# Kernel tuning notes

Measured on AMD Instinct MI355X. Metric: run time of the kernel, lower is better.

Reference implementation:

```python
import jax, jax.numpy as jnp
import numpy as np

S, R, NUM_LORA = 16384, 64, 8
NQ, NKV = 4096, 1024
OUT_DIM = NQ + 2 * NKV
BS, MAX_LEN = 32, 512


def setup_inputs() -> dict:
    key = jax.random.key(0)
    k1, k2, k3, k4, k5, k6 = jax.random.split(key, 6)
    x = jax.random.normal(k1, (S, 3 * R), dtype=jnp.float32)
    qkv_lora_b = jax.random.normal(k2, (NUM_LORA, OUT_DIM, R), dtype=jnp.float32) * 0.02
    seg_indptr = (jnp.arange(BS + 1, dtype=jnp.int32) * MAX_LEN)
    seg_lens = jax.random.randint(k3, (BS,), 256, MAX_LEN + 1, dtype=jnp.int32)
    weight_indices = jax.random.randint(k4, (BS,), 0, NUM_LORA, dtype=jnp.int32)
    # ranks in [0, R]; rank 0 means the segment is a no-op
    lora_ranks = jax.random.randint(k5, (NUM_LORA,), 0, R + 1, dtype=jnp.int32)
    scalings = jax.random.uniform(k6, (NUM_LORA,), minval=0.25, maxval=2.0, dtype=jnp.float32)
    output_offset = jnp.array([0, NQ, NQ + NKV, OUT_DIM], dtype=jnp.int32)
    return {
        "x": x,
        "qkv_lora_b": qkv_lora_b,
        "use_cuda_graph": False,
        "bs": BS,
        "num_segments": BS,
        "seg_indptr": seg_indptr,
        "weight_indices": weight_indices,
        "lora_ranks": lora_ranks,
        "scalings": scalings,
        "max_len": MAX_LEN,
        "seg_lens": seg_lens,
        "permutation": jnp.arange(BS, dtype=jnp.int32),
        "output_offset": output_offset,
        "max_qkv_out_dim": NQ,
    }


def _qkv_lora_b(x, qkv_lora_b, bs, seg_indptr, weight_indices, lora_ranks,
                scalings, max_len, seg_lens, offs):
    s = x.shape[0]
    out_dim, r = qkv_lora_b.shape[1], qkv_lora_b.shape[2]
    L = max_len
    w_idx = weight_indices[:bs]                      # (bs,)
    W = qkv_lora_b[w_idx]                            # (bs, out_dim, r)
    keff = jnp.minimum(r, lora_ranks[w_idx])         # effective rank per segment
    scale = scalings[w_idx]                          # (bs,)
    # gather padded per-segment token blocks
    pos = seg_indptr[:bs, None] + jnp.arange(L, dtype=seg_indptr.dtype)[None, :]   # (bs, L)
    valid = jnp.arange(L)[None, :] < seg_lens[:bs, None]                            # (bs, L)
    Xp = jnp.where(valid[..., None], x[jnp.clip(pos, 0, s - 1)], 0.0)               # (bs, L, 3r)
    # x columns for qkv slice q are [q*keff, q*keff + keff) (packed with stride keff)
    kidx = jnp.arange(r, dtype=jnp.int32)
    cols = jnp.arange(3, dtype=jnp.int32)[None, :, None] * keff[:, None, None] + kidx[None, None, :]  # (bs,3,r)
    kmask = kidx[None, None, :] < keff[:, None, None]
    cols = jnp.where(kmask, cols, 0)
    Xg = jnp.take_along_axis(Xp[:, :, None, :],
                             jnp.broadcast_to(cols[:, None], (bs, L, 3, r)), axis=3)  # (bs, L, 3, r)
    Xg = Xg * kmask[:, None].astype(Xg.dtype)
    # 3 packed GEMMs against the statically-partitioned B weight (Q / K / V rows)
    parts = [jnp.einsum('blk,bnk->bln', Xg[:, :, q], W[:, offs[q]:offs[q + 1], :])
             for q in range(3)]
    seg_out = jnp.concatenate(parts, axis=-1) * scale[:, None, None]    # (bs, L, out_dim)
    # masked scatter-add back into the flat output buffer
    pos_safe = jnp.where(valid, pos, s)   # out-of-range index -> dropped
    out = jnp.zeros((s, out_dim), dtype=x.dtype)
    out = out.at[pos_safe.reshape(-1)].add(seg_out.reshape(-1, out_dim), mode='drop')
    return out


def reference(x, qkv_lora_b, use_cuda_graph, bs, num_segments, seg_indptr,
              weight_indices, lora_ranks, scalings, max_len, seg_lens,
              permutation, output_offset, max_qkv_out_dim):
    offs = np.asarray(jax.device_get(output_offset))  # static [0, Nq, Nq+Nkv, out_dim]
    return _qkv_lora_b(x, qkv_lora_b, int(bs), seg_indptr, weight_indices,
                       lora_ranks, scalings, int(max_len), seg_lens, offs)
```

## Files before the change

### kernel.cpp

```cpp
#include <hip/hip_runtime.h>
#include <stddef.h>

#define SROWS   16384
#define ODIM    6144
#define RMAX    64
#define SEGLEN  512
#define TM      64
#define TN      128
#define XDIM    192

typedef float f4_t __attribute__((ext_vector_type(4)));

__global__ __launch_bounds__(256, 3) void lora_qkv_b_kernel(
    const float* __restrict__ x,
    const float* __restrict__ w_all,
    const int*   __restrict__ weight_indices,
    const int*   __restrict__ lora_ranks,
    const float* __restrict__ scalings,
    const int*   __restrict__ seg_lens,
    float*       __restrict__ out)
{
    __shared__ float xs[TM][RMAX];
    __shared__ float wlds[RMAX][TN + 4];

    const int seg   = blockIdx.x;
    const int cb    = blockIdx.y;
    const int half  = blockIdx.z;
    const int n0    = cb * TN;
    const int segbase = seg * SEGLEN;
    const int lbase = half * (SEGLEN / 2);

    const int w    = weight_indices[seg];
    int keff       = lora_ranks[w];
    if (keff > RMAX) keff = RMAX;
    const float scale = scalings[w];
    const int slen    = seg_lens[seg];

    const int tid    = threadIdx.x;
    const int rbase  = (tid >> 5) * 8;
    const int nlocal = (tid & 31) * 4;

    if (keff == 0 || lbase >= slen) {
        const f4_t z = (f4_t)0.f;
        for (int c = 0; c < 4; ++c) {
            const int i0 = segbase + lbase + c * TM;
            #pragma unroll
            for (int r = 0; r < 8; ++r)
                __builtin_nontemporal_store(
                    z, (f4_t*)(out + (size_t)(i0 + rbase + r) * ODIM + n0 + nlocal));
        }
        return;
    }

    const int q    = (n0 < 4096) ? 0 : ((n0 < 5120) ? 1 : 2);
    const int qoff = q * keff;
    const float* Wb = w_all + ((size_t)w * ODIM + n0) * RMAX;

    for (int idx = tid * 4; idx < TN * RMAX; idx += 256 * 4) {
        const int n  = idx >> 6;
        const int k0 = idx & 63;
        float4 v = make_float4(0.f, 0.f, 0.f, 0.f);
        if (k0 < keff) {
            v = *(const float4*)(Wb + (size_t)n * RMAX + k0);
            if (k0 + 1 >= keff) v.y = 0.f;
            if (k0 + 2 >= keff) v.z = 0.f;
            if (k0 + 3 >= keff) v.w = 0.f;
        }
        wlds[k0 + 0][n] = v.x;
        wlds[k0 + 1][n] = v.y;
        wlds[k0 + 2][n] = v.z;
        wlds[k0 + 3][n] = v.w;
    }

    const int kk = tid & 63;
    const int r0 = tid >> 6;
    const int keff4 = (keff + 3) & ~3;

    float pref[16];
    {
        const float* p = x + ((size_t)(segbase + lbase) + r0) * XDIM + qoff + kk;
        #pragma unroll
        for (int m = 0; m < 16; ++m) pref[m] = p[(size_t)m * 4 * XDIM];
    }

    for (int c = 0; c < 4; ++c) {
        const int l0 = lbase + c * TM;
        const int i0 = segbase + l0;

        if (l0 >= slen) {
            const f4_t z = (f4_t)0.f;
            #pragma unroll
            for (int r = 0; r < 8; ++r)
                __builtin_nontemporal_store(
                    z, (f4_t*)(out + (size_t)(i0 + rbase + r) * ODIM + n0 + nlocal));
            continue;
        }

        if (l0 + TM <= slen) {
            #pragma unroll
            for (int m = 0; m < 16; ++m) xs[m * 4 + r0][kk] = pref[m];
        } else {
            #pragma unroll
            for (int m = 0; m < 16; ++m)
                xs[m * 4 + r0][kk] = (l0 + m * 4 + r0 < slen) ? pref[m] : 0.f;
        }

        __syncthreads();

        if (c < 3 && l0 + TM < slen) {
            const float* p = x + ((size_t)(i0 + TM) + r0) * XDIM + qoff + kk;
            #pragma unroll
            for (int m = 0; m < 16; ++m) pref[m] = p[(size_t)m * 4 * XDIM];
        }

        float acc[8][4];
        #pragma unroll
        for (int r = 0; r < 8; ++r)
            #pragma unroll
            for (int cc = 0; cc < 4; ++cc) acc[r][cc] = 0.f;

        for (int k = 0; k < keff4; k += 4) {
            const float4 w0 = *(const float4*)(&wlds[k + 0][nlocal]);
            const float4 w1 = *(const float4*)(&wlds[k + 1][nlocal]);
            const float4 w2 = *(const float4*)(&wlds[k + 2][nlocal]);
            const float4 w3 = *(const float4*)(&wlds[k + 3][nlocal]);
            #pragma unroll
            for (int r = 0; r < 8; ++r) {
                const float4 xv = *(const float4*)(&xs[rbase + r][k]);
                acc[r][0] += xv.x * w0.x; acc[r][1] += xv.x * w0.y;
                acc[r][2] += xv.x * w0.z; acc[r][3] += xv.x * w0.w;
                acc[r][0] += xv.y * w1.x; acc[r][1] += xv.y * w1.y;
                acc[r][2] += xv.y * w1.z; acc[r][3] += xv.y * w1.w;
                acc[r][0] += xv.z * w2.x; acc[r][1] += xv.z * w2.y;
                acc[r][2] += xv.z * w2.z; acc[r][3] += xv.z * w2.w;
                acc[r][0] += xv.w * w3.x; acc[r][1] += xv.w * w3.y;
                acc[r][2] += xv.w * w3.z; acc[r][3] += xv.w * w3.w;
            }
        }

        __syncthreads();

        #pragma unroll
        for (int r = 0; r < 8; ++r) {
            const size_t row = (size_t)(i0 + rbase + r);
            f4_t o;
            o.x = acc[r][0] * scale;
            o.y = acc[r][1] * scale;
            o.z = acc[r][2] * scale;
            o.w = acc[r][3] * scale;
            __builtin_nontemporal_store(o, (f4_t*)(out + row * ODIM + n0 + nlocal));
        }
    }
}

extern "C" void kernel_launch(void* const* d_in, const int* in_sizes, int n_in,
                              void* d_out, int out_size, void* d_ws, size_t ws_size,
                              hipStream_t stream) {
    const float* x    = (const float*)d_in[0];
    const float* wb   = (const float*)d_in[1];
    const int*   widx = (const int*)d_in[6];
    const int*   rks  = (const int*)d_in[7];
    const float* scl  = (const float*)d_in[8];
    const int*   sln  = (const int*)d_in[10];
    float* out = (float*)d_out;

    dim3 grid(32, ODIM / TN, 2);
    lora_qkv_b_kernel<<<grid, 256, 0, stream>>>(x, wb, widx, rks, scl, sln, out);
}
```

Measured before the change: 483.7 us.

## Load x directly from global with register double-buffering, drop LDS staging

Removes the shared-memory staging tile for x and the per-chunk barriers around it. Each thread now reads its eight x rows straight from global memory as unaligned 4-wide vectors and double-buffers both the x and weight fragments across 8-wide k steps. Masking of rows past the segment length moves from the input staging to the output scaling. The trade-off is redundant global or cache reads of x across lanes, unaligned vector loads, and padding the rank to a multiple of 8 instead of 4.

```diff
diff --git a/kernel.cpp b/kernel.cpp
--- a/kernel.cpp
+++ b/kernel.cpp
@@ -9,7 +9,8 @@
 #define TN      128
 #define XDIM    192
 
-typedef float f4_t __attribute__((ext_vector_type(4)));
+typedef float f4_t  __attribute__((ext_vector_type(4)));
+typedef float f4u_t __attribute__((ext_vector_type(4), aligned(4)));
 
 __global__ __launch_bounds__(256, 3) void lora_qkv_b_kernel(
     const float* __restrict__ x,
@@ -20,7 +21,6 @@
     const int*   __restrict__ seg_lens,
     float*       __restrict__ out)
 {
-    __shared__ float xs[TM][RMAX];
     __shared__ float wlds[RMAX][TN + 4];
 
     const int seg   = blockIdx.x;
@@ -72,16 +72,9 @@
         wlds[k0 + 3][n] = v.w;
     }
 
-    const int kk = tid & 63;
-    const int r0 = tid >> 6;
-    const int keff4 = (keff + 3) & ~3;
+    __syncthreads();
 
-    float pref[16];
-    {
-        const float* p = x + ((size_t)(segbase + lbase) + r0) * XDIM + qoff + kk;
-        #pragma unroll
-        for (int m = 0; m < 16; ++m) pref[m] = p[(size_t)m * 4 * XDIM];
-    }
+    const int nk8 = (keff + 7) >> 3;
 
     for (int c = 0; c < 4; ++c) {
         const int l0 = lbase + c * TM;
@@ -96,59 +89,88 @@
             continue;
         }
 
-        if (l0 + TM <= slen) {
-            #pragma unroll
-            for (int m = 0; m < 16; ++m) xs[m * 4 + r0][kk] = pref[m];
-        } else {
-            #pragma unroll
-            for (int m = 0; m < 16; ++m)
-                xs[m * 4 + r0][kk] = (l0 + m * 4 + r0 < slen) ? pref[m] : 0.f;
-        }
+        const float* xb = x + (size_t)(i0 + rbase) * XDIM + qoff;
 
-        __syncthreads();
+        f4u_t xA[8], xB[8];
+        f4_t  wA[4], wB[4];
 
-        if (c < 3 && l0 + TM < slen) {
-            const float* p = x + ((size_t)(i0 + TM) + r0) * XDIM + qoff + kk;
-            #pragma unroll
-            for (int m = 0; m < 16; ++m) pref[m] = p[(size_t)m * 4 * XDIM];
-        }
+        #pragma unroll
+        for (int r = 0; r < 8; ++r) xA[r] = *(const f4u_t*)(xb + r * XDIM + 0);
+        #pragma unroll
+        for (int j = 0; j < 4; ++j) wA[j] = *(const f4_t*)(&wlds[0 + j][nlocal]);
+        #pragma unroll
+        for (int r = 0; r < 8; ++r) xB[r] = *(const f4u_t*)(xb + r * XDIM + 4);
+        #pragma unroll
+        for (int j = 0; j < 4; ++j) wB[j] = *(const f4_t*)(&wlds[4 + j][nlocal]);
 
         float acc[8][4];
         #pragma unroll
-        for (int r = 0; r < 8; ++r)
-            #pragma unroll
-            for (int cc = 0; cc < 4; ++cc) acc[r][cc] = 0.f;
+        for (int r = 0; r < 8; ++r) {
+            acc[r][0] = 0.f; acc[r][1] = 0.f; acc[r][2] = 0.f; acc[r][3] = 0.f;
+        }
 
-        for (int k = 0; k < keff4; k += 4) {
-            const float4 w0 = *(const float4*)(&wlds[k + 0][nlocal]);
-            const float4 w1 = *(const float4*)(&wlds[k + 1][nlocal]);
-            const float4 w2 = *(const float4*)(&wlds[k + 2][nlocal]);
-            const float4 w3 = *(const float4*)(&wlds[k + 3][nlocal]);
+        for (int g = 0; ; ++g) {
             #pragma unroll
             for (int r = 0; r < 8; ++r) {
-                const float4 xv = *(const float4*)(&xs[rbase + r][k]);
-                acc[r][0] += xv.x * w0.x; acc[r][1] += xv.x * w0.y;
-                acc[r][2] += xv.x * w0.z; acc[r][3] += xv.x * w0.w;
-                acc[r][0] += xv.y * w1.x; acc[r][1] += xv.y * w1.y;
-                acc[r][2] += xv.y * w1.z; acc[r][3] += xv.y * w1.w;
-                acc[r][0] += xv.z * w2.x; acc[r][1] += xv.z * w2.y;
-                acc[r][2] += xv.z * w2.z; acc[r][3] += xv.z * w2.w;
-                acc[r][0] += xv.w * w3.x; acc[r][1] += xv.w * w3.y;
-                acc[r][2] += xv.w * w3.z; acc[r][3] += xv.w * w3.w;
+                const f4u_t xv = xA[r];
+                acc[r][0] += xv.x * wA[0].x; acc[r][1] += xv.x * wA[0].y;
+                acc[r][2] += xv.x * wA[0].z; acc[r][3] += xv.x * wA[0].w;
+                acc[r][0] += xv.y * wA[1].x; acc[r][1] += xv.y * wA[1].y;
+                acc[r][2] += xv.y * wA[1].z; acc[r][3] += xv.y * wA[1].w;
+                acc[r][0] += xv.z * wA[2].x; acc[r][1] += xv.z * wA[2].y;
+                acc[r][2] += xv.z * wA[2].z; acc[r][3] += xv.z * wA[2].w;
+                acc[r][0] += xv.w * wA[3].x; acc[r][1] += xv.w * wA[3].y;
+                acc[r][2] += xv.w * wA[3].z; acc[r][3] += xv.w * wA[3].w;
+            }
+            const bool more = (g + 1 < nk8);
+            if (more) {
+                const int kn = 8 * g + 8;
+                #pragma unroll
+                for (int r = 0; r < 8; ++r) xA[r] = *(const f4u_t*)(xb + r * XDIM + kn);
+                #pragma unroll
+                for (int j = 0; j < 4; ++j) wA[j] = *(const f4_t*)(&wlds[kn + j][nlocal]);
+            }
+            #pragma unroll
+            for (int r = 0; r < 8; ++r) {
+                const f4u_t xv = xB[r];
+                acc[r][0] += xv.x * wB[0].x; acc[r][1] += xv.x * wB[0].y;
+                acc[r][2] += xv.x * wB[0].z; acc[r][3] += xv.x * wB[0].w;
+                acc[r][0] += xv.y * wB[1].x; acc[r][1] += xv.y * wB[1].y;
+                acc[r][2] += xv.y * wB[1].z; acc[r][3] += xv.y * wB[1].w;
+                acc[r][0] += xv.z * wB[2].x; acc[r][1] += xv.z * wB[2].y;
+                acc[r][2] += xv.z * wB[2].z; acc[r][3] += xv.z * wB[2].w;
+                acc[r][0] += xv.w * wB[3].x; acc[r][1] += xv.w * wB[3].y;
+                acc[r][2] += xv.w * wB[3].z; acc[r][3] += xv.w * wB[3].w;
+            }
+            if (!more) break;
+            {
+                const int kn = 8 * g + 12;
+                #pragma unroll
+                for (int r = 0; r < 8; ++r) xB[r] = *(const f4u_t*)(xb + r * XDIM + kn);
+                #pragma unroll
+                for (int j = 0; j < 4; ++j) wB[j] = *(const f4_t*)(&wlds[kn + j][nlocal]);
             }
         }
 
-        __syncthreads();
-
-        #pragma unroll
-        for (int r = 0; r < 8; ++r) {
-            const size_t row = (size_t)(i0 + rbase + r);
-            f4_t o;
-            o.x = acc[r][0] * scale;
-            o.y = acc[r][1] * scale;
-            o.z = acc[r][2] * scale;
-            o.w = acc[r][3] * scale;
-            __builtin_nontemporal_store(o, (f4_t*)(out + row * ODIM + n0 + nlocal));
+        if (l0 + TM <= slen) {
+            #pragma unroll
+            for (int r = 0; r < 8; ++r) {
+                f4_t o;
+                o.x = acc[r][0] * scale; o.y = acc[r][1] * scale;
+                o.z = acc[r][2] * scale; o.w = acc[r][3] * scale;
+                __builtin_nontemporal_store(
+                    o, (f4_t*)(out + (size_t)(i0 + rbase + r) * ODIM + n0 + nlocal));
+            }
+        } else {
+            #pragma unroll
+            for (int r = 0; r < 8; ++r) {
+                const float m = (l0 + rbase + r < slen) ? scale : 0.f;
+                f4_t o;
+                o.x = acc[r][0] * m; o.y = acc[r][1] * m;
+                o.z = acc[r][2] * m; o.w = acc[r][3] * m;
+                __builtin_nontemporal_store(
+                    o, (f4_t*)(out + (size_t)(i0 + rbase + r) * ODIM + n0 + nlocal));
+            }
         }
     }
 }
```

New measurement: 843.6 us. +74.4%, slower.
